# Kernel tuning notes

Measured on AMD Instinct MI355X. Metric: run time of the kernel, lower is better.

The kernel has to match this reference:

```python
import jax, jax.numpy as jnp
import numpy as np
import math

B, N, D, H = 4, 2048, 512, 8
DK = D // H


def setup_inputs() -> dict:
    key = jax.random.key(0)
    ks = jax.random.split(key, 7)
    s = 1.0 / math.sqrt(D)
    return {
        "Q": jax.random.normal(ks[0], (B, N, D), jnp.float32),
        "K": jax.random.normal(ks[1], (B, N, D), jnp.float32),
        "V": jax.random.normal(ks[2], (B, N, D), jnp.float32),
        "Wq": jax.random.normal(ks[3], (D, D), jnp.float32) * s,
        "bq": jax.random.normal(ks[4], (D,), jnp.float32) * s,
        "Wo": jax.random.normal(ks[5], (D, D), jnp.float32) * s,
        "bo": jax.random.normal(ks[6], (D,), jnp.float32) * s,
    }


def _split_heads(x):
    b, n, _ = x.shape
    return x.reshape(b, n, H, DK).transpose(0, 2, 1, 3)  # [B,H,N,dk]


def reference(Q, K, V, Wq, bq, Wo, bo):
    # Faithful to source: W_q projects Q, K, AND V (source bug kept).
    proj = lambda x: jnp.einsum("bnd,ed->bne", x, Wq) + bq
    q = _split_heads(proj(Q))
    k = _split_heads(proj(K))
    v = _split_heads(proj(V))
    scores = jnp.einsum("bhnd,bhmd->bhnm", q, k) / math.sqrt(DK)  # [B,H,N,N]
    # Faithful to source: softmax over dim=1 == the HEADS axis.
    probs = jax.nn.softmax(scores, axis=1)
    A = jnp.einsum("bhnm,bhmd->bhnd", probs, v)  # [B,H,N,dk]
    A = A.transpose(0, 2, 1, 3).reshape(B, N, D)  # combine heads
    return jnp.einsum("bnd,ed->bne", A, Wo) + bo
```

## Files before the change

### kernel.cpp

```cpp
#include <hip/hip_runtime.h>
#include <hip/hip_bf16.h>

#define B_  4
#define N_  2048
#define D_  512
#define H_  8

typedef unsigned short u16;
typedef __attribute__((ext_vector_type(8))) unsigned short ushort8;
typedef __attribute__((ext_vector_type(4))) unsigned short us4;
typedef __attribute__((ext_vector_type(8))) short short8;
typedef __attribute__((ext_vector_type(4))) float float4v;

__device__ __forceinline__ float bf2f(u16 u) {
    union { unsigned int i; float f; } v;
    v.i = ((unsigned int)u) << 16;
    return v.f;
}
__device__ __forceinline__ u16 f2bf(float f) {
    union { float f; unsigned int i; } v;
    v.f = f;
    unsigned int r = v.i + 0x7FFFu + ((v.i >> 16) & 1u);
    return (u16)(r >> 16);
}
__device__ __forceinline__ u16 f2bf_fast(float f) {
    union { float f; unsigned int i; } v;
    v.f = f;
    return (u16)((v.i + 0x8000u) >> 16);
}

__device__ __forceinline__ void gload_lds16(const void* g, void* l) {
    __builtin_amdgcn_global_load_lds(
        (const __attribute__((address_space(1))) unsigned int*)g,
        (__attribute__((address_space(3))) unsigned int*)l, 16, 0, 0);
}

__global__ __launch_bounds__(256) void wconv(
    const float* __restrict__ Wq, const float* __restrict__ Wo,
    u16* __restrict__ out)
{
    const int idx = (blockIdx.x * 256 + threadIdx.x) * 8;
    const float* src = blockIdx.y ? Wo : Wq;
    u16* dst = out + (size_t)blockIdx.y * (D_ * D_) + idx;
    float4v a = *(const float4v*)(src + idx);
    float4v b = *(const float4v*)(src + idx + 4);
    ushort8 o;
    #pragma unroll
    for (int j = 0; j < 4; ++j) { o[j] = f2bf(a[j]); o[j + 4] = f2bf(b[j]); }
    *(ushort8*)dst = o;
}

__global__ __launch_bounds__(256) void cvt3(
    const float* __restrict__ Q, const float* __restrict__ K,
    const float* __restrict__ V, u16* __restrict__ out)
{
    const size_t NBD = (size_t)B_ * N_ * D_;
    const float* src = (blockIdx.y == 0) ? Q : ((blockIdx.y == 1) ? K : V);
    u16* dst = out + (size_t)blockIdx.y * NBD;
    size_t idx = ((size_t)blockIdx.x * 256 + threadIdx.x) * 8;
    float4v a = *(const float4v*)(src + idx);
    float4v b = *(const float4v*)(src + idx + 4);
    ushort8 o;
    #pragma unroll
    for (int j = 0; j < 4; ++j) { o[j] = f2bf(a[j]); o[j + 4] = f2bf(b[j]); }
    *(ushort8*)(dst + idx) = o;
}

template <int INK, bool WB16, bool OUTB16, int NZ>
__global__ __launch_bounds__(256) void proj_mfma(
    const void* __restrict__ X0v, const void* __restrict__ X1v,
    const void* __restrict__ X2v, const void* __restrict__ Wv,
    const float* __restrict__ bias, void* __restrict__ C0v, int M)
{
    __shared__ u16 As[128][32];
    __shared__ u16 Bs[128][32];

    const int t = threadIdx.x;
    const int flat = blockIdx.x;
    const int xcd = flat & 7, rr = flat >> 3;
    const int eb = rr & 3, g = rr >> 2;
    const int zm = xcd + 8 * g;
    const int z  = zm >> 6;
    const int e0 = eb * 128;
    const int m0 = (zm & 63) * 128;

    const void* Xv = (z == 0) ? X0v : ((z == 1) ? X1v : X2v);
    const int w = t >> 6, l = t & 63;
    const int lane16 = l & 15, quad = l >> 4;
    const int wr = (w >> 1) * 64;
    const int wc = (w & 1) * 64;

    float4v acc[4][4];
    #pragma unroll
    for (int i = 0; i < 4; ++i)
        #pragma unroll
        for (int j = 0; j < 4; ++j)
            acc[i][j] = (float4v){0.f, 0.f, 0.f, 0.f};

    for (int k0 = 0; k0 < 512; k0 += 32) {
        __syncthreads();

        if (INK == 1) {
            const u16* X = (const u16*)Xv;
            #pragma unroll
            for (int i = 0; i < 2; ++i) {
                int r0 = w * 32 + i * 16;
                gload_lds16(X + (size_t)(m0 + r0 + (l >> 2)) * 512 + k0 + (l & 3) * 8,
                            &As[r0][0]);
            }
        } else if (INK == 0) {
            const float* X = (const float*)Xv;
            #pragma unroll
            for (int i = 0; i < 2; ++i) {
                int v   = t + 256 * i;
                int row = v >> 2;
                int c8  = (v & 3) * 8;
                const float* xp = X + (size_t)(m0 + row) * 512 + k0 + c8;
                float4v x0 = *(const float4v*)xp;
                float4v x1 = *(const float4v*)(xp + 4);
                ushort8 o;
                #pragma unroll
                for (int j = 0; j < 4; ++j) {
                    o[j]     = f2bf_fast(x0[j]);
                    o[j + 4] = f2bf_fast(x1[j]);
                }
                *(ushort8*)&As[row][c8] = o;
            }
        } else {
            const u16* P0 = (const u16*)X0v;
            const u16* P1 = (const u16*)X1v;
            #pragma unroll
            for (int i = 0; i < 2; ++i) {
                int v   = t + 256 * i;
                int row = v >> 2;
                int c8  = (v & 3) * 8;
                size_t gi = (size_t)(m0 + row) * 512 + k0 + c8;
                ushort8 a = *(const ushort8*)(P0 + gi);
                ushort8 b = *(const ushort8*)(P1 + gi);
                ushort8 o;
                #pragma unroll
                for (int j = 0; j < 8; ++j) o[j] = f2bf(bf2f(a[j]) + bf2f(b[j]));
                *(ushort8*)&As[row][c8] = o;
            }
        }

        if (WB16) {
            const u16* Wb = (const u16*)Wv;
            #pragma unroll
            for (int i = 0; i < 2; ++i) {
                int r0 = w * 32 + i * 16;
                gload_lds16(Wb + (size_t)(e0 + r0 + (l >> 2)) * 512 + k0 + (l & 3) * 8,
                            &Bs[r0][0]);
            }
        } else {
            const float* W = (const float*)Wv;
            #pragma unroll
            for (int i = 0; i < 2; ++i) {
                int v   = t + 256 * i;
                int row = v >> 2;
                int c8  = (v & 3) * 8;
                const float* wp = W + (size_t)(e0 + row) * 512 + k0 + c8;
                float4v w0 = *(const float4v*)wp;
                float4v w1 = *(const float4v*)(wp + 4);
                ushort8 o;
                #pragma unroll
                for (int j = 0; j < 4; ++j) {
                    o[j]     = f2bf_fast(w0[j]);
                    o[j + 4] = f2bf_fast(w1[j]);
                }
                *(ushort8*)&Bs[row][c8] = o;
            }
        }
        __syncthreads();

        short8 af[4], bfr[4];
        #pragma unroll
        for (int i = 0; i < 4; ++i)
            af[i] = *(const short8*)&As[wr + i * 16 + lane16][quad * 8];
        #pragma unroll
        for (int j = 0; j < 4; ++j)
            bfr[j] = *(const short8*)&Bs[wc + j * 16 + lane16][quad * 8];
        #pragma unroll
        for (int i = 0; i < 4; ++i)
            #pragma unroll
            for (int j = 0; j < 4; ++j)
                acc[i][j] = __builtin_amdgcn_mfma_f32_16x16x32_bf16(
                    af[i], bfr[j], acc[i][j], 0, 0, 0);
    }

    float bj[4];
    #pragma unroll
    for (int j = 0; j < 4; ++j) bj[j] = bias[e0 + wc + j * 16 + lane16];

    if (OUTB16) {
        if (z == 2) {
            u16* C = (u16*)C0v + 2 * (size_t)M * D_;
            #pragma unroll
            for (int i = 0; i < 4; ++i) {
                int mrow = m0 + wr + i * 16 + quad * 4;
                int bb = mrow >> 11, nb = mrow & (N_ - 1);
                #pragma unroll
                for (int j = 0; j < 4; ++j) {
                    int e = e0 + wc + j * 16 + lane16;
                    us4 o;
                    #pragma unroll
                    for (int r = 0; r < 4; ++r) o[r] = f2bf(acc[i][j][r] + bj[j]);
                    *(us4*)(C + (size_t)(bb * D_ + e) * N_ + nb) = o;
                }
            }
        } else {
            u16* C = (u16*)C0v + (size_t)z * (size_t)M * D_;
            #pragma unroll
            for (int i = 0; i < 4; ++i)
                #pragma unroll
                for (int j = 0; j < 4; ++j) {
                    int e = e0 + wc + j * 16 + lane16;
                    #pragma unroll
                    for (int r = 0; r < 4; ++r) {
                        int mrow = m0 + wr + i * 16 + quad * 4 + r;
                        C[(size_t)mrow * D_ + e] = f2bf(acc[i][j][r] + bj[j]);
                    }
                }
        }
    } else {
        float* C = (float*)C0v;
        #pragma unroll
        for (int i = 0; i < 4; ++i)
            #pragma unroll
            for (int j = 0; j < 4; ++j) {
                int e = e0 + wc + j * 16 + lane16;
                #pragma unroll
                for (int r = 0; r < 4; ++r) {
                    int mrow = m0 + wr + i * 16 + quad * 4 + r;
                    C[(size_t)mrow * D_ + e] = acc[i][j][r] + bj[j];
                }
            }
    }
}

__global__ __launch_bounds__(512, 2) void attn_mfma4(
    const u16* __restrict__ Qp, const u16* __restrict__ Kp,
    const u16* __restrict__ Vpt, u16* __restrict__ A0)
{
    __shared__ u16 Ks[32][520];
    __shared__ u16 Vs[512][40];
    __shared__ u16 Ps[4][8][16][40];

    const int t = threadIdx.x;
    const int w = t >> 6, l = t & 63;
    const int lane16 = l & 15, quad = l >> 4;
    const int ns = w >> 1, ms = w & 1;

    const int flat = blockIdx.x;
    const int xcd  = flat & 7;
    const int b = xcd >> 1;
    const int z = xcd & 1;
    const int n0 = (flat >> 3) * 64 + ns * 16;
    const int seg  = N_ / 2;
    const int mbeg = z * seg;
    u16* A = A0 + (size_t)z * ((size_t)B_ * N_ * D_);

    short8 qfrag[8][2];
    {
        const u16* qb = Qp + ((size_t)(b * N_ + n0 + lane16) * D_ + quad * 8);
        #pragma unroll
        for (int h = 0; h < 8; ++h)
            #pragma unroll
            for (int dc = 0; dc < 2; ++dc)
                qfrag[h][dc] = *(const short8*)(qb + h * 64 + dc * 32);
    }

    float4v aacc[8][2];
    #pragma unroll
    for (int h = 0; h < 8; ++h)
        #pragma unroll
        for (int dt = 0; dt < 2; ++dt)
            aacc[h][dt] = (float4v){0.f, 0.f, 0.f, 0.f};

    for (int mc = mbeg; mc < mbeg + seg; mc += 32) {
        __syncthreads();

        #pragma unroll
        for (int i = 0; i < 4; ++i) {
            int row = w * 4 + i;
            gload_lds16(Kp + (size_t)(b * N_ + mc + row) * D_ + l * 8, &Ks[row][0]);
        }
        #pragma unroll
        for (int i = 0; i < 4; ++i) {
            int v = i * 512 + t;
            int d = v >> 2, part = v & 3;
            ushort8 x = *(const ushort8*)(Vpt + (size_t)(b * D_ + d) * N_ + mc + part * 8);
            *(ushort8*)&Vs[d][part * 8] = x;
        }
        __syncthreads();

        {
            float4v sacc[8];
            #pragma unroll
            for (int h = 0; h < 8; ++h) sacc[h] = (float4v){0.f, 0.f, 0.f, 0.f};
            #pragma unroll
            for (int h = 0; h < 8; ++h)
                #pragma unroll
                for (int dc = 0; dc < 2; ++dc) {
                    short8 kf = *(const short8*)
                        &Ks[ms * 16 + lane16][h * 64 + dc * 32 + quad * 8];
                    sacc[h] = __builtin_amdgcn_mfma_f32_16x16x32_bf16(
                        qfrag[h][dc], kf, sacc[h], 0, 0, 0);
                }
            #pragma unroll
            for (int r = 0; r < 4; ++r) {
                float p[8]; float sum = 0.f;
                #pragma unroll
                for (int h = 0; h < 8; ++h) {
                    p[h] = __expf(sacc[h][r] * 0.125f);
                    sum += p[h];
                }
                float inv = 1.f / sum;
                #pragma unroll
                for (int h = 0; h < 8; ++h)
                    Ps[ns][h][quad * 4 + r][ms * 16 + lane16] = f2bf(p[h] * inv);
            }
        }
        __syncthreads();

        #pragma unroll
        for (int h = 0; h < 8; ++h) {
            short8 pf = *(const short8*)&Ps[ns][h][lane16][quad * 8];
            #pragma unroll
            for (int dt = 0; dt < 2; ++dt) {
                short8 vf = *(const short8*)
                    &Vs[h * 64 + (ms * 2 + dt) * 16 + lane16][quad * 8];
                aacc[h][dt] = __builtin_amdgcn_mfma_f32_16x16x32_bf16(
                    pf, vf, aacc[h][dt], 0, 0, 0);
            }
        }
    }

    #pragma unroll
    for (int h = 0; h < 8; ++h)
        #pragma unroll
        for (int dt = 0; dt < 2; ++dt)
            #pragma unroll
            for (int r = 0; r < 4; ++r) {
                const int n = n0 + quad * 4 + r;
                const int d = h * 64 + (ms * 2 + dt) * 16 + lane16;
                A[(size_t)(b * N_ + n) * D_ + d] = f2bf(aacc[h][dt][r]);
            }
}

extern "C" void kernel_launch(void* const* d_in, const int* in_sizes, int n_in,
                              void* d_out, int out_size, void* d_ws, size_t ws_size,
                              hipStream_t stream)
{
    const float* Q  = (const float*)d_in[0];
    const float* K  = (const float*)d_in[1];
    const float* V  = (const float*)d_in[2];
    const float* Wq = (const float*)d_in[3];
    const float* bq = (const float*)d_in[4];
    const float* Wo = (const float*)d_in[5];
    const float* bo = (const float*)d_in[6];
    float* out = (float*)d_out;
    u16*   ws  = (u16*)d_ws;

    const size_t NBD = (size_t)B_ * N_ * D_;
    const int M = B_ * N_;

    const size_t need6 = (6 * NBD + 2 * (size_t)D_ * D_) * sizeof(u16);

    if (ws_size >= need6) {
        u16* S0 = ws;
        u16* S1 = ws + NBD;
        u16* S2 = ws + 2 * NBD;
        u16* S3 = ws + 3 * NBD;
        u16* Wb = ws + 6 * NBD;

        cvt3<<<dim3((unsigned)(NBD / 2048), 3), dim3(256), 0, stream>>>(Q, K, V, S0);
        wconv<<<dim3(128, 2), dim3(256), 0, stream>>>(Wq, Wo, Wb);

        proj_mfma<1, true, true, 3><<<dim3(768), dim3(256), 0, stream>>>(
            S0, S1, S2, Wb, bq, S3, M);

        attn_mfma4<<<dim3(256), dim3(512), 0, stream>>>(
            S3, S3 + NBD, S3 + 2 * NBD, S0);

        proj_mfma<2, true, false, 1><<<dim3(256), dim3(256), 0, stream>>>(
            S0, S1, S1, Wb + (size_t)D_ * D_, bo, out, M);
    } else {
        u16* Qp  = ws;
        u16* Kp  = ws + NBD;
        u16* Vpt = ws + 2 * NBD;
        u16* Pa  = ws + 3 * NBD;
        u16* Pb  = ws + 4 * NBD;
        u16* Wb  = ws + 5 * NBD;

        wconv<<<dim3(128, 2), dim3(256), 0, stream>>>(Wq, Wo, Wb);

        proj_mfma<0, true, true, 3><<<dim3(768), dim3(256), 0, stream>>>(
            Q, K, V, Wb, bq, Qp, M);

        attn_mfma4<<<dim3(256), dim3(512), 0, stream>>>(Qp, Kp, Vpt, Pa);

        proj_mfma<2, true, false, 1><<<dim3(256), dim3(256), 0, stream>>>(
            Pa, Pb, Pb, Wb + (size_t)D_ * D_, bo, out, M);
    }
}
```

Measured before the change: 275.6 us.

## Double-buffer K tiles in LDS and read V fragments directly from global

The attention kernel now double-buffers the K tile in shared memory, prefetching the next chunk with async global-to-LDS loads while the current chunk's P·V MFMAs run. V is no longer staged through LDS; each lane loads its V fragment straight from the transposed global buffer. It also uses a hardware reciprocal for the softmax normaliser, raises wave priority around MFMA sections, and shrinks the padding on the P buffer. The aim is to hide load latency and cut one barrier per iteration, at the cost of uncoalesced, L2-dependent V reads, possible LDS bank conflicts from the new P stride, and slightly less precise normalisation.

```diff
diff --git a/kernel.cpp b/kernel.cpp
--- a/kernel.cpp
+++ b/kernel.cpp
@@ -238,13 +238,12 @@
     }
 }
 
-__global__ __launch_bounds__(512, 2) void attn_mfma4(
+__global__ __launch_bounds__(512, 2) void attn_mfma5(
     const u16* __restrict__ Qp, const u16* __restrict__ Kp,
     const u16* __restrict__ Vpt, u16* __restrict__ A0)
 {
-    __shared__ u16 Ks[32][520];
-    __shared__ u16 Vs[512][40];
-    __shared__ u16 Ps[4][8][16][40];
+    __shared__ u16 Ks[2][32][520];
+    __shared__ u16 Ps[4][8][16][36];
 
     const int t = threadIdx.x;
     const int w = t >> 6, l = t & 63;
@@ -260,6 +259,9 @@
     const int mbeg = z * seg;
     u16* A = A0 + (size_t)z * ((size_t)B_ * N_ * D_);
 
+    const u16* Kb = Kp  + (size_t)b * N_ * D_;
+    const u16* Vb = Vpt + ((size_t)(b * D_ + ms * 32 + lane16)) * N_ + quad * 8;
+
     short8 qfrag[8][2];
     {
         const u16* qb = Qp + ((size_t)(b * N_ + n0 + lane16) * D_ + quad * 8);
@@ -277,63 +279,71 @@
         for (int dt = 0; dt < 2; ++dt)
             aacc[h][dt] = (float4v){0.f, 0.f, 0.f, 0.f};
 
-    for (int mc = mbeg; mc < mbeg + seg; mc += 32) {
+    #pragma unroll
+    for (int i = 0; i < 4; ++i) {
+        int row = w * 4 + i;
+        gload_lds16(Kb + (size_t)(mbeg + row) * D_ + l * 8, &Ks[0][row][0]);
+    }
+    __syncthreads();
+
+    const int nch = seg / 32;
+    for (int c = 0; c < nch; ++c) {
+        const int cur = c & 1;
+        const int mc  = mbeg + c * 32;
+
+        float4v sacc[8];
+        #pragma unroll
+        for (int h = 0; h < 8; ++h) sacc[h] = (float4v){0.f, 0.f, 0.f, 0.f};
+        __builtin_amdgcn_s_setprio(1);
+        #pragma unroll
+        for (int h = 0; h < 8; ++h)
+            #pragma unroll
+            for (int dc = 0; dc < 2; ++dc) {
+                short8 kf = *(const short8*)
+                    &Ks[cur][ms * 16 + lane16][h * 64 + dc * 32 + quad * 8];
+                sacc[h] = __builtin_amdgcn_mfma_f32_16x16x32_bf16(
+                    qfrag[h][dc], kf, sacc[h], 0, 0, 0);
+            }
+        __builtin_amdgcn_s_setprio(0);
+
+        #pragma unroll
+        for (int r = 0; r < 4; ++r) {
+            float p[8]; float sum = 0.f;
+            #pragma unroll
+            for (int h = 0; h < 8; ++h) {
+                p[h] = __expf(sacc[h][r] * 0.125f);
+                sum += p[h];
+            }
+            float inv = __builtin_amdgcn_rcpf(sum);
+            #pragma unroll
+            for (int h = 0; h < 8; ++h)
+                Ps[ns][h][quad * 4 + r][ms * 16 + lane16] = f2bf(p[h] * inv);
+        }
         __syncthreads();
 
-        #pragma unroll
-        for (int i = 0; i < 4; ++i) {
-            int row = w * 4 + i;
-            gload_lds16(Kp + (size_t)(b * N_ + mc + row) * D_ + l * 8, &Ks[row][0]);
-        }
-        #pragma unroll
-        for (int i = 0; i < 4; ++i) {
-            int v = i * 512 + t;
-            int d = v >> 2, part = v & 3;
-            ushort8 x = *(const ushort8*)(Vpt + (size_t)(b * D_ + d) * N_ + mc + part * 8);
-            *(ushort8*)&Vs[d][part * 8] = x;
-        }
-        __syncthreads();
-
-        {
-            float4v sacc[8];
-            #pragma unroll
-            for (int h = 0; h < 8; ++h) sacc[h] = (float4v){0.f, 0.f, 0.f, 0.f};
-            #pragma unroll
-            for (int h = 0; h < 8; ++h)
-                #pragma unroll
-                for (int dc = 0; dc < 2; ++dc) {
-                    short8 kf = *(const short8*)
-                        &Ks[ms * 16 + lane16][h * 64 + dc * 32 + quad * 8];
-                    sacc[h] = __builtin_amdgcn_mfma_f32_16x16x32_bf16(
-                        qfrag[h][dc], kf, sacc[h], 0, 0, 0);
-                }
-            #pragma unroll
-            for (int r = 0; r < 4; ++r) {
-                float p[8]; float sum = 0.f;
-                #pragma unroll
-                for (int h = 0; h < 8; ++h) {
-                    p[h] = __expf(sacc[h][r] * 0.125f);
-                    sum += p[h];
-                }
-                float inv = 1.f / sum;
-                #pragma unroll
-                for (int h = 0; h < 8; ++h)
-                    Ps[ns][h][quad * 4 + r][ms * 16 + lane16] = f2bf(p[h] * inv);
-            }
-        }
-        __syncthreads();
-
+        if (c + 1 < nch) {
+            #pragma unroll
+            for (int i = 0; i < 4; ++i) {
+                int row = w * 4 + i;
+                gload_lds16(Kb + (size_t)(mc + 32 + row) * D_ + l * 8,
+                            &Ks[cur ^ 1][row][0]);
+            }
+        }
+
+        __builtin_amdgcn_s_setprio(1);
         #pragma unroll
         for (int h = 0; h < 8; ++h) {
             short8 pf = *(const short8*)&Ps[ns][h][lane16][quad * 8];
             #pragma unroll
             for (int dt = 0; dt < 2; ++dt) {
                 short8 vf = *(const short8*)
-                    &Vs[h * 64 + (ms * 2 + dt) * 16 + lane16][quad * 8];
+                    (Vb + (size_t)(h * 64 + dt * 16) * N_ + mc);
                 aacc[h][dt] = __builtin_amdgcn_mfma_f32_16x16x32_bf16(
                     pf, vf, aacc[h][dt], 0, 0, 0);
             }
         }
+        __builtin_amdgcn_s_setprio(0);
+        __syncthreads();
     }
 
     #pragma unroll
@@ -380,7 +390,7 @@
         proj_mfma<1, true, true, 3><<<dim3(768), dim3(256), 0, stream>>>(
             S0, S1, S2, Wb, bq, S3, M);
 
-        attn_mfma4<<<dim3(256), dim3(512), 0, stream>>>(
+        attn_mfma5<<<dim3(256), dim3(512), 0, stream>>>(
             S3, S3 + NBD, S3 + 2 * NBD, S0);
 
         proj_mfma<2, true, false, 1><<<dim3(256), dim3(256), 0, stream>>>(
@@ -398,7 +408,7 @@
         proj_mfma<0, true, true, 3><<<dim3(768), dim3(256), 0, stream>>>(
             Q, K, V, Wb, bq, Qp, M);
 
-        attn_mfma4<<<dim3(256), dim3(512), 0, stream>>>(Qp, Kp, Vpt, Pa);
+        attn_mfma5<<<dim3(256), dim3(512), 0, stream>>>(Qp, Kp, Vpt, Pa);
 
         proj_mfma<2, true, false, 1><<<dim3(256), dim3(256), 0, stream>>>(
             Pa, Pb, Pb, Wb + (size_t)D_ * D_, bo, out, M);
```

After: 335.8 us. +21.8%, slower.
